# Performance work log

Hardware: AMD Instinct MI355X
Metric: run time of the kernel (lower is better)

Reference implementation:

```python
import jax, jax.numpy as jnp
import numpy as np

D_MODEL = 1024
N_HEADS = 16
HIDDEN = int(D_MODEL * 4 * 2 / 3)  # 2730, matches torch int(d*4*2/3)
EPS = 1e-6


def setup_inputs() -> dict:
    key = jax.random.key(0)
    ks = jax.random.split(key, 8)
    B, T = 4, 2048
    s = 0.02
    return {
        "x": jax.random.normal(ks[0], (B, T, D_MODEL), dtype=jnp.float32),
        "w_attn": jax.random.normal(ks[1], (D_MODEL, 3 * D_MODEL), dtype=jnp.float32) * s,
        "w_proj": jax.random.normal(ks[2], (D_MODEL, D_MODEL), dtype=jnp.float32) * s,
        "w1": jax.random.normal(ks[3], (D_MODEL, HIDDEN), dtype=jnp.float32) * s,
        "w2": jax.random.normal(ks[4], (D_MODEL, HIDDEN), dtype=jnp.float32) * s,
        "w3": jax.random.normal(ks[5], (HIDDEN, D_MODEL), dtype=jnp.float32) * s,
        "g1": jnp.ones((D_MODEL,), dtype=jnp.float32),
        "g2": jnp.ones((D_MODEL,), dtype=jnp.float32),
    }


def rmsnorm(x, g):
    norm = jax.lax.rsqrt(jnp.mean(x * x, axis=-1, keepdims=True) + EPS)
    return x * norm * g


def reference(x, w_attn, w_proj, w1, w2, w3, g1, g2):
    B, T, C = x.shape
    H = N_HEADS
    hd = C // H

    # attention branch
    qkv = rmsnorm(x, g1) @ w_attn                     # [B,T,3C]
    q, k, v = jnp.split(qkv, 3, axis=-1)
    q = q.reshape(B, T, H, hd).transpose(0, 2, 1, 3)  # [B,H,T,hd]
    k = k.reshape(B, T, H, hd).transpose(0, 2, 1, 3)
    v = v.reshape(B, T, H, hd).transpose(0, 2, 1, 3)

    att = jnp.einsum("bhqd,bhkd->bhqk", q, k) / jnp.sqrt(jnp.float32(hd))
    causal = jnp.tril(jnp.ones((T, T), dtype=bool))
    att = jnp.where(causal[None, None], att, jnp.float32(-jnp.inf))
    att = jax.nn.softmax(att, axis=-1)
    y = jnp.einsum("bhqk,bhkd->bhqd", att, v)          # [B,H,T,hd]
    y = y.transpose(0, 2, 1, 3).reshape(B, T, C)
    attn_out = y @ w_proj

    # parallel MLP branch on ln_2(x) (note: applied to x, not x+attn)
    h = rmsnorm(x, g2)
    mlp_out = (jax.nn.silu(h @ w1) * (h @ w2)) @ w3

    # dropout is identity in eval mode
    return x + attn_out + mlp_out
```

## Files before the change

kernel.cpp:

```cpp
#include <hip/hip_runtime.h>

#define TT 2048
#define DM 1024
#define HPAD 2816
#define HID 2730

typedef __attribute__((ext_vector_type(4))) float f32x4;
typedef __attribute__((ext_vector_type(8))) short bf16x8;

static __device__ __forceinline__ float bf2f(short u) {
    union { float f; unsigned int i; } c; c.i = ((unsigned int)(unsigned short)u) << 16; return c.f;
}
static __device__ __forceinline__ short f2bf(float f) {
    union { float f; unsigned int i; } c; c.f = f;
    unsigned int i = c.i;
    unsigned int r = (i + 0x7fffu + ((i >> 16) & 1u)) >> 16;
    return (short)r;
}

static __device__ __forceinline__ void gload_lds16(const void* g, void* l) {
    __builtin_amdgcn_global_load_lds(
        (const __attribute__((address_space(1))) unsigned int*)g,
        (__attribute__((address_space(3))) unsigned int*)l, 16, 0, 0);
}

__global__ __launch_bounds__(256) void wprep(const float* __restrict__ in, short* __restrict__ out,
                                             int K, int N, int Kpad, int Npad) {
    __shared__ float tile[32][33];
    int kb = blockIdx.x * 32, nb = blockIdx.y * 32;
    int tx = threadIdx.x, ty = threadIdx.y;
    #pragma unroll
    for (int i = 0; i < 32; i += 8) {
        int k = kb + ty + i, n = nb + tx;
        float v = (k < K && n < N) ? in[(size_t)k * N + n] : 0.f;
        tile[tx][ty + i] = v;
    }
    __syncthreads();
    #pragma unroll
    for (int i = 0; i < 32; i += 8) {
        int n = nb + ty + i, k = kb + tx;
        if (n < Npad && k < Kpad) out[(size_t)n * Kpad + k] = f2bf(tile[ty + i][tx]);
    }
}

__global__ __launch_bounds__(256) void rmsnorm2(const float* __restrict__ x,
    const float* __restrict__ g1, const float* __restrict__ g2,
    short* __restrict__ xn1, short* __restrict__ xn2) {
    int row = blockIdx.x;
    const float* xr = x + (size_t)row * DM;
    int t = threadIdx.x;
    float4 v = ((const float4*)xr)[t];
    float ss = v.x*v.x + v.y*v.y + v.z*v.z + v.w*v.w;
    #pragma unroll
    for (int off = 1; off < 64; off <<= 1) ss += __shfl_xor(ss, off);
    __shared__ float red[4];
    if ((t & 63) == 0) red[t >> 6] = ss;
    __syncthreads();
    float tot = red[0] + red[1] + red[2] + red[3];
    float rs = rsqrtf(tot * (1.0f / DM) + 1e-6f);
    float4 G1 = ((const float4*)g1)[t];
    float4 G2 = ((const float4*)g2)[t];
    union { short s[4]; int2 v; } o1, o2;
    o1.s[0] = f2bf(v.x * rs * G1.x); o1.s[1] = f2bf(v.y * rs * G1.y);
    o1.s[2] = f2bf(v.z * rs * G1.z); o1.s[3] = f2bf(v.w * rs * G1.w);
    o2.s[0] = f2bf(v.x * rs * G2.x); o2.s[1] = f2bf(v.y * rs * G2.y);
    o2.s[2] = f2bf(v.z * rs * G2.z); o2.s[3] = f2bf(v.w * rs * G2.w);
    *(int2*)(xn1 + (size_t)row * DM + t * 4) = o1.v;
    *(int2*)(xn2 + (size_t)row * DM + t * 4) = o2.v;
}

template<int EPI>
__global__ __launch_bounds__(256) void gemm_bt(
    const short* __restrict__ A, const short* __restrict__ Bt,
    short* __restrict__ Cb, const float* __restrict__ X, float* __restrict__ Of,
    int M, int N, int K)
{
    __shared__ short As[128 * 64];
    __shared__ short Bs[128 * 64];
    int t = threadIdx.x;
    int wid = t >> 6, l = t & 63;
    int wm = wid >> 1, wn = wid & 1;

    int nwg = gridDim.x, bid = blockIdx.x;
    int wg = (bid & 7) * (nwg >> 3) + (bid >> 3);
    int tiles_n = N >> 7;
    int tm = wg / tiles_n, tn = wg % tiles_n;

    const short* Arow = A + (size_t)(tm * 128) * K;
    const short* Brow = Bt + (size_t)(tn * 128) * K;

    f32x4 acc[4][4];
    #pragma unroll
    for (int m = 0; m < 4; m++)
        #pragma unroll
        for (int n = 0; n < 4; n++) acc[m][n] = (f32x4){0.f, 0.f, 0.f, 0.f};

    for (int kt = 0; kt < K; kt += 64) {
        __syncthreads();
        #pragma unroll
        for (int i = 0; i < 4; i++) {
            int linear = i * 256 + t;
            int row = linear >> 3;
            int slot = linear & 7;
            int srcslot = slot ^ (row & 7);
            gload_lds16(Arow + (size_t)row * K + kt + srcslot * 8, (char*)As + linear * 16);
            gload_lds16(Brow + (size_t)row * K + kt + srcslot * 8, (char*)Bs + linear * 16);
        }
        __syncthreads();
        #pragma unroll
        for (int ks = 0; ks < 2; ks++) {
            bf16x8 af[4], bfr[4];
            #pragma unroll
            for (int m = 0; m < 4; m++) {
                int row = wm * 64 + m * 16 + (l & 15);
                af[m] = *(const bf16x8*)((char*)As + row * 128 + ((ks * 64 + (l >> 4) * 16) ^ ((row & 7) << 4)));
            }
            #pragma unroll
            for (int n = 0; n < 4; n++) {
                int row = wn * 64 + n * 16 + (l & 15);
                bfr[n] = *(const bf16x8*)((char*)Bs + row * 128 + ((ks * 64 + (l >> 4) * 16) ^ ((row & 7) << 4)));
            }
            #pragma unroll
            for (int m = 0; m < 4; m++)
                #pragma unroll
                for (int n = 0; n < 4; n++)
                    acc[m][n] = __builtin_amdgcn_mfma_f32_16x16x32_bf16(af[m], bfr[n], acc[m][n], 0, 0, 0);
        }
    }

    #pragma unroll
    for (int m = 0; m < 4; m++)
        #pragma unroll
        for (int n = 0; n < 4; n++)
            #pragma unroll
            for (int r = 0; r < 4; r++) {
                int row = tm * 128 + wm * 64 + m * 16 + (l >> 4) * 4 + r;
                int col = tn * 128 + wn * 64 + n * 16 + (l & 15);
                size_t idx = (size_t)row * N + col;
                float v = acc[m][n][r];
                if constexpr (EPI == 0) Cb[idx] = f2bf(v);
                else if constexpr (EPI == 1) Of[idx] = X[idx] + v;
                else if constexpr (EPI == 4) Of[idx] += v;
            }
}

__global__ __launch_bounds__(512, 2) void gemm_mlp2(
    const short* __restrict__ A, const short* __restrict__ B1t, const short* __restrict__ B2t,
    short* __restrict__ Cb, int M, int N, int K)
{
    __shared__ short As[128 * 64];
    __shared__ short B1s[128 * 64];
    __shared__ short B2s[128 * 64];
    int t = threadIdx.x;
    int wid = t >> 6, l = t & 63;
    int wm = wid >> 2, wn = wid & 3;

    int nwg = gridDim.x, bid = blockIdx.x;
    int wg = (bid & 7) * (nwg >> 3) + (bid >> 3);
    int tiles_n = N >> 7;
    int tm = wg / tiles_n, tn = wg % tiles_n;

    const short* Arow  = A   + (size_t)(tm * 128) * K;
    const short* B1row = B1t + (size_t)(tn * 128) * K;
    const short* B2row = B2t + (size_t)(tn * 128) * K;

    f32x4 acc1[4][2], acc2[4][2];
    #pragma unroll
    for (int m = 0; m < 4; m++)
        #pragma unroll
        for (int n = 0; n < 2; n++) {
            acc1[m][n] = (f32x4){0.f, 0.f, 0.f, 0.f};
            acc2[m][n] = (f32x4){0.f, 0.f, 0.f, 0.f};
        }

    for (int kt = 0; kt < K; kt += 64) {
        __syncthreads();
        #pragma unroll
        for (int i = 0; i < 2; i++) {
            int linear = i * 512 + t;
            int row = linear >> 3;
            int slot = linear & 7;
            int srcslot = slot ^ (row & 7);
            gload_lds16(Arow  + (size_t)row * K + kt + srcslot * 8, (char*)As  + linear * 16);
            gload_lds16(B1row + (size_t)row * K + kt + srcslot * 8, (char*)B1s + linear * 16);
            gload_lds16(B2row + (size_t)row * K + kt + srcslot * 8, (char*)B2s + linear * 16);
        }
        __syncthreads();
        #pragma unroll
        for (int ks = 0; ks < 2; ks++) {
            bf16x8 af[4], b1[2], b2[2];
            #pragma unroll
            for (int m = 0; m < 4; m++) {
                int row = wm * 64 + m * 16 + (l & 15);
                int off = (ks * 64 + (l >> 4) * 16) ^ ((row & 7) << 4);
                af[m] = *(const bf16x8*)((char*)As + row * 128 + off);
            }
            #pragma unroll
            for (int n = 0; n < 2; n++) {
                int row = wn * 32 + n * 16 + (l & 15);
                int off = (ks * 64 + (l >> 4) * 16) ^ ((row & 7) << 4);
                b1[n] = *(const bf16x8*)((char*)B1s + row * 128 + off);
                b2[n] = *(const bf16x8*)((char*)B2s + row * 128 + off);
            }
            #pragma unroll
            for (int m = 0; m < 4; m++)
                #pragma unroll
                for (int n = 0; n < 2; n++) {
                    acc1[m][n] = __builtin_amdgcn_mfma_f32_16x16x32_bf16(af[m], b1[n], acc1[m][n], 0, 0, 0);
                    acc2[m][n] = __builtin_amdgcn_mfma_f32_16x16x32_bf16(af[m], b2[n], acc2[m][n], 0, 0, 0);
                }
        }
    }

    #pragma unroll
    for (int m = 0; m < 4; m++)
        #pragma unroll
        for (int n = 0; n < 2; n++)
            #pragma unroll
            for (int r = 0; r < 4; r++) {
                int row = tm * 128 + wm * 64 + m * 16 + (l >> 4) * 4 + r;
                int col = tn * 128 + wn * 32 + n * 16 + (l & 15);
                float v1 = acc1[m][n][r];
                float v2 = acc2[m][n][r];
                Cb[(size_t)row * N + col] = f2bf(v1 * (1.f / (1.f + __expf(-v1))) * v2);
            }
}

#define PSTR 76
#define SM_C 0.18033688f
__global__ __launch_bounds__(512, 4) void attn(const short* __restrict__ qkv, short* __restrict__ y) {
    __shared__ short Ks[2][64 * 64];
    __shared__ short Vt[2][64 * 64];
    __shared__ short Ps[8][16 * PSTR];
    int bid = blockIdx.x;
    int xcd = bid & 7;
    int idx = bid >> 3;
    int bh  = xcd + 8 * (idx >> 3);
    int pair = idx & 7;
    int b = bh >> 4, h = bh & 15;
    int t = threadIdx.x, wid = t >> 6, l = t & 63;
    const size_t base = (size_t)b * TT * 3072;

    int krow = t >> 3, kslot = t & 7, ksrc = kslot ^ (krow & 7);
    int vrow = t >> 3, vch = t & 7;

    #pragma unroll
    for (int pass = 0; pass < 2; pass++) {
        int qt = pass == 0 ? (15 - pair) : pair;
        int q0 = qt * 128 + wid * 16;

        bf16x8 qf[2];
        #pragma unroll
        for (int s = 0; s < 2; s++) {
            int row = q0 + (l & 15);
            qf[s] = *(const bf16x8*)(qkv + base + (size_t)row * 3072 + h * 64 + s * 32 + (l >> 4) * 8);
        }

        f32x4 o[4];
        #pragma unroll
        for (int n = 0; n < 4; n++) o[n] = (f32x4){0.f, 0.f, 0.f, 0.f};
        float ll[4];
        #pragma unroll
        for (int r = 0; r < 4; r++) ll[r] = 0.f;

        int nt = 2 * qt + 2;

        {
            gload_lds16(qkv + base + (size_t)krow * 3072 + 1024 + h * 64 + ksrc * 8,
                        (char*)Ks + t * 16);
            uint4 vv = *(const uint4*)(qkv + base + (size_t)vrow * 3072 + 2048 + h * 64 + vch * 8);
            const short* vs = (const short*)&vv;
            #pragma unroll
            for (int j = 0; j < 8; j++) {
                int d = vch * 8 + j;
                int byte = (d * 128 + vrow * 2) ^ (((j ^ vch) & 7) << 4);
                *(short*)((char*)Vt + byte) = vs[j];
            }
            __syncthreads();
        }

        int cur = 0;
        for (int it = 0; it < nt; ++it) {
            int kb = it << 6;
            bool have_next = (it + 1 < nt);
            uint4 vv;
            if (have_next) {
                int nkb = kb + 64;
                gload_lds16(qkv + base + (size_t)(nkb + krow) * 3072 + 1024 + h * 64 + ksrc * 8,
                            (char*)Ks + (cur ^ 1) * 8192 + t * 16);
                vv = *(const uint4*)(qkv + base + (size_t)(nkb + vrow) * 3072 + 2048 + h * 64 + vch * 8);
            }
            if (kb <= q0 + 15) {
                f32x4 s4[4];
                __builtin_amdgcn_s_setprio(1);
                #pragma unroll
                for (int j = 0; j < 4; j++) {
                    f32x4 z = (f32x4){0.f, 0.f, 0.f, 0.f};
                    #pragma unroll
                    for (int ks = 0; ks < 2; ks++) {
                        int row = j * 16 + (l & 15);
                        bf16x8 kf = *(const bf16x8*)((char*)Ks + cur * 8192 + row * 128 +
                                    ((ks * 64 + (l >> 4) * 16) ^ ((row & 7) << 4)));
                        z = __builtin_amdgcn_mfma_f32_16x16x32_bf16(qf[ks], kf, z, 0, 0, 0);
                    }
                    s4[j] = z;
                }
                __builtin_amdgcn_s_setprio(0);
                bool diag = (kb + 63 > q0);
                #pragma unroll
                for (int j = 0; j < 4; j++)
                    #pragma unroll
                    for (int r = 0; r < 4; r++) {
                        float v = s4[j][r];
                        if (diag) {
                            int qrow = q0 + (l >> 4) * 4 + r;
                            int kcol = kb + j * 16 + (l & 15);
                            if (kcol > qrow) v = -3e38f;
                        }
                        float p = exp2f(v * SM_C);
                        s4[j][r] = p;
                        ll[r] += p;
                    }

                short* P = &Ps[wid][0];
                #pragma unroll
                for (int j = 0; j < 4; j++)
                    #pragma unroll
                    for (int r = 0; r < 4; r++)
                        P[((l >> 4) * 4 + r) * PSTR + j * 16 + (l & 15)] = f2bf(s4[j][r]);

                bf16x8 pf[2];
                #pragma unroll
                for (int ks = 0; ks < 2; ks++)
                    pf[ks] = *(const bf16x8*)(P + (l & 15) * PSTR + ks * 32 + (l >> 4) * 8);
                __builtin_amdgcn_s_setprio(1);
                #pragma unroll
                for (int n = 0; n < 4; n++) {
                    #pragma unroll
                    for (int ks = 0; ks < 2; ks++) {
                        int vr = n * 16 + (l & 15);
                        int f = (vr & 7) ^ ((vr >> 3) & 7);
                        bf16x8 vf = *(const bf16x8*)((char*)Vt + cur * 8192 + vr * 128 +
                                    ((ks * 64 + (l >> 4) * 16) ^ (f << 4)));
                        o[n] = __builtin_amdgcn_mfma_f32_16x16x32_bf16(pf[ks], vf, o[n], 0, 0, 0);
                    }
                }
                __builtin_amdgcn_s_setprio(0);
            }
            if (have_next) {
                const short* vs = (const short*)&vv;
                #pragma unroll
                for (int j = 0; j < 8; j++) {
                    int d = vch * 8 + j;
                    int byte = (d * 128 + vrow * 2) ^ (((j ^ vch) & 7) << 4);
                    *(short*)((char*)Vt + (cur ^ 1) * 8192 + byte) = vs[j];
                }
            }
            __syncthreads();
            cur ^= 1;
        }

        #pragma unroll
        for (int r = 0; r < 4; r++) {
            #pragma unroll
            for (int off = 1; off < 16; off <<= 1) ll[r] += __shfl_xor(ll[r], off);
        }
        float inv[4];
        #pragma unroll
        for (int r = 0; r < 4; r++) inv[r] = 1.f / ll[r];
        #pragma unroll
        for (int n = 0; n < 4; n++)
            #pragma unroll
            for (int r = 0; r < 4; r++) {
                int row = q0 + (l >> 4) * 4 + r;
                int col = h * 64 + n * 16 + (l & 15);
                y[(size_t)(b * TT + row) * DM + col] = f2bf(o[n][r] * inv[r]);
            }
    }
}

extern "C" void kernel_launch(void* const* d_in, const int* in_sizes, int n_in,
                              void* d_out, int out_size, void* d_ws, size_t ws_size,
                              hipStream_t stream) {
    (void)in_sizes; (void)n_in; (void)out_size; (void)ws_size;
    const float* x      = (const float*)d_in[0];
    const float* w_attn = (const float*)d_in[1];
    const float* w_proj = (const float*)d_in[2];
    const float* w1     = (const float*)d_in[3];
    const float* w2     = (const float*)d_in[4];
    const float* w3     = (const float*)d_in[5];
    const float* g1     = (const float*)d_in[6];
    const float* g2     = (const float*)d_in[7];
    float* out = (float*)d_out;

    char* ws = (char*)d_ws;
    size_t off = 0;
    auto alloc = [&](size_t bytes) { char* p = ws + off; off += (bytes + 255) & ~(size_t)255; return p; };
    short* wattn_t = (short*)alloc((size_t)3072 * 1024 * 2);
    short* wproj_t = (short*)alloc((size_t)1024 * 1024 * 2);
    short* w1t     = (short*)alloc((size_t)HPAD * 1024 * 2);
    short* w2t     = (short*)alloc((size_t)HPAD * 1024 * 2);
    short* w3t     = (short*)alloc((size_t)1024 * HPAD * 2);
    short* xn1     = (short*)alloc((size_t)8192 * 1024 * 2);
    short* xn2     = (short*)alloc((size_t)8192 * 1024 * 2);
    short* qkvb    = (short*)alloc((size_t)8192 * 3072 * 2);
    short* yb      = (short*)alloc((size_t)8192 * 1024 * 2);
    short* hb      = (short*)alloc((size_t)8192 * HPAD * 2);

    dim3 tb(32, 8);
    wprep<<<dim3(32, 96), tb, 0, stream>>>(w_attn, wattn_t, 1024, 3072, 1024, 3072);
    wprep<<<dim3(32, 32), tb, 0, stream>>>(w_proj, wproj_t, 1024, 1024, 1024, 1024);
    wprep<<<dim3(32, 88), tb, 0, stream>>>(w1, w1t, 1024, HID, 1024, HPAD);
    wprep<<<dim3(32, 88), tb, 0, stream>>>(w2, w2t, 1024, HID, 1024, HPAD);
    wprep<<<dim3(88, 32), tb, 0, stream>>>(w3, w3t, HID, 1024, HPAD, 1024);

    rmsnorm2<<<8192, 256, 0, stream>>>(x, g1, g2, xn1, xn2);

    gemm_bt<0><<<1536, 256, 0, stream>>>(xn1, wattn_t, qkvb, nullptr, nullptr, 8192, 3072, 1024);
    attn<<<512, 512, 0, stream>>>(qkvb, yb);
    gemm_bt<1><<<512, 256, 0, stream>>>(yb, wproj_t, nullptr, x, out, 8192, 1024, 1024);
    gemm_mlp2<<<1408, 512, 0, stream>>>(xn2, w1t, w2t, hb, 8192, HPAD, 1024);
    gemm_bt<4><<<512, 256, 0, stream>>>(hb, w3t, nullptr, nullptr, out, 8192, 1024, HPAD);
}
```

Measured before the change: 384.0 us.

## Fuse output projection and MLP down-projection GEMMs; prescale Q and truncate P

```diff
diff --git a/kernel.cpp b/kernel.cpp
--- a/kernel.cpp
+++ b/kernel.cpp
@@ -16,6 +16,10 @@
     unsigned int i = c.i;
     unsigned int r = (i + 0x7fffu + ((i >> 16) & 1u)) >> 16;
     return (short)r;
+}
+static __device__ __forceinline__ short f2bf_trunc(float f) {
+    union { float f; unsigned int i; } c; c.f = f;
+    return (short)(c.i >> 16);
 }
 
 static __device__ __forceinline__ void gload_lds16(const void* g, void* l) {
@@ -144,6 +148,80 @@
             }
 }
 
+__global__ __launch_bounds__(256) void gemm_fuse(
+    const short* __restrict__ A1, const short* __restrict__ B1,
+    const short* __restrict__ A2, const short* __restrict__ B2,
+    const float* __restrict__ X, float* __restrict__ Of)
+{
+    __shared__ short As[128 * 64];
+    __shared__ short Bs[128 * 64];
+    int t = threadIdx.x;
+    int wid = t >> 6, l = t & 63;
+    int wm = wid >> 1, wn = wid & 1;
+
+    int nwg = gridDim.x, bid = blockIdx.x;
+    int wg = (bid & 7) * (nwg >> 3) + (bid >> 3);
+    int tiles_n = 8;
+    int tm = wg / tiles_n, tn = wg % tiles_n;
+
+    f32x4 acc[4][4];
+    #pragma unroll
+    for (int m = 0; m < 4; m++)
+        #pragma unroll
+        for (int n = 0; n < 4; n++) acc[m][n] = (f32x4){0.f, 0.f, 0.f, 0.f};
+
+    #pragma unroll 1
+    for (int phase = 0; phase < 2; phase++) {
+        const short* Arow = phase == 0 ? A1 + (size_t)(tm * 128) * 1024 : A2 + (size_t)(tm * 128) * HPAD;
+        const short* Brow = phase == 0 ? B1 + (size_t)(tn * 128) * 1024 : B2 + (size_t)(tn * 128) * HPAD;
+        int K = phase == 0 ? 1024 : HPAD;
+        for (int kt = 0; kt < K; kt += 64) {
+            __syncthreads();
+            #pragma unroll
+            for (int i = 0; i < 4; i++) {
+                int linear = i * 256 + t;
+                int row = linear >> 3;
+                int slot = linear & 7;
+                int srcslot = slot ^ (row & 7);
+                gload_lds16(Arow + (size_t)row * K + kt + srcslot * 8, (char*)As + linear * 16);
+                gload_lds16(Brow + (size_t)row * K + kt + srcslot * 8, (char*)Bs + linear * 16);
+            }
+            __syncthreads();
+            #pragma unroll
+            for (int ks = 0; ks < 2; ks++) {
+                bf16x8 af[4], bfr[4];
+                #pragma unroll
+                for (int m = 0; m < 4; m++) {
+                    int row = wm * 64 + m * 16 + (l & 15);
+                    af[m] = *(const bf16x8*)((char*)As + row * 128 + ((ks * 64 + (l >> 4) * 16) ^ ((row & 7) << 4)));
+                }
+                #pragma unroll
+                for (int n = 0; n < 4; n++) {
+                    int row = wn * 64 + n * 16 + (l & 15);
+                    bfr[n] = *(const bf16x8*)((char*)Bs + row * 128 + ((ks * 64 + (l >> 4) * 16) ^ ((row & 7) << 4)));
+                }
+                #pragma unroll
+                for (int m = 0; m < 4; m++)
+                    #pragma unroll
+                    for (int n = 0; n < 4; n++)
+                        acc[m][n] = __builtin_amdgcn_mfma_f32_16x16x32_bf16(af[m], bfr[n], acc[m][n], 0, 0, 0);
+            }
+        }
+    }
+
+    #pragma unroll
+    for (int m = 0; m < 4; m++)
+        #pragma unroll
+        for (int n = 0; n < 4; n++)
+            #pragma unroll
+            for (int r = 0; r < 4; r++) {
+                int row = tm * 128 + wm * 64 + m * 16 + (l >> 4) * 4 + r;
+                int col = tn * 128 + wn * 64 + n * 16 + (l & 15);
+                size_t idx = (size_t)row * 1024 + col;
+                Of[idx] = X[idx] + acc[m][n][r];
+            }
+}
+
 __global__ __launch_bounds__(512, 2) void gemm_mlp2(
     const short* __restrict__ A, const short* __restrict__ B1t, const short* __restrict__ B2t,
     short* __restrict__ Cb, int M, int N, int K)
@@ -253,7 +331,10 @@
         #pragma unroll
         for (int s = 0; s < 2; s++) {
             int row = q0 + (l & 15);
-            qf[s] = *(const bf16x8*)(qkv + base + (size_t)row * 3072 + h * 64 + s * 32 + (l >> 4) * 8);
+            bf16x8 q = *(const bf16x8*)(qkv + base + (size_t)row * 3072 + h * 64 + s * 32 + (l >> 4) * 8);
+            #pragma unroll
+            for (int i = 0; i < 8; i++) q[i] = f2bf(bf2f(q[i]) * SM_C);
+            qf[s] = q;
         }
 
         f32x4 o[4];
@@ -317,7 +398,7 @@
                             int kcol = kb + j * 16 + (l & 15);
                             if (kcol > qrow) v = -3e38f;
                         }
-                        float p = exp2f(v * SM_C);
+                        float p = exp2f(v);
                         s4[j][r] = p;
                         ll[r] += p;
                     }
@@ -327,7 +408,7 @@
                 for (int j = 0; j < 4; j++)
                     #pragma unroll
                     for (int r = 0; r < 4; r++)
-                        P[((l >> 4) * 4 + r) * PSTR + j * 16 + (l & 15)] = f2bf(s4[j][r]);
+                        P[((l >> 4) * 4 + r) * PSTR + j * 16 + (l & 15)] = f2bf_trunc(s4[j][r]);
 
                 bf16x8 pf[2];
                 #pragma unroll
@@ -418,7 +499,6 @@
 
     gemm_bt<0><<<1536, 256, 0, stream>>>(xn1, wattn_t, qkvb, nullptr, nullptr, 8192, 3072, 1024);
     attn<<<512, 512, 0, stream>>>(qkvb, yb);
-    gemm_bt<1><<<512, 256, 0, stream>>>(yb, wproj_t, nullptr, x, out, 8192, 1024, 1024);
     gemm_mlp2<<<1408, 512, 0, stream>>>(xn2, w1t, w2t, hb, 8192, HPAD, 1024);
-    gemm_bt<4><<<512, 256, 0, stream>>>(hb, w3t, nullptr, nullptr, out, 8192, 1024, HPAD);
-}
+    gemm_fuse<<<512, 256, 0, stream>>>(yb, wproj_t, hb, w3t, x, out);
+}
```

New measurement: 357.8 us. 6.8% less time.
